# Performance work log

Hardware: AMD Instinct MI355X
Metric: run time of the kernel (lower is better)

Reference implementation:

```python
import jax, jax.numpy as jnp
import numpy as np

NUM_Q_HEADS = 64
NUM_KV_HEADS = 8
HEAD_DIM = 64
HIDDEN = 2880
SLIDING_WINDOW = 128
ROPE_WAVELENGTH = 10000.0
NEG_INF = jnp.float32(-1e9)


def _rope(x, start_index=0):
    # x: (b, s, n, h). yarn with scaling_factor=1.0 == standard RoPE (split-half rotate).
    s, h = x.shape[1], x.shape[-1]
    inv_freq = 1.0 / (ROPE_WAVELENGTH ** (jnp.arange(0, h, 2, dtype=jnp.float32) / h))
    pos = jnp.arange(s, dtype=jnp.float32) + start_index
    freqs = pos[:, None] * inv_freq[None, :]  # (s, h/2)
    cos = jnp.concatenate([jnp.cos(freqs), jnp.cos(freqs)], axis=-1)[None, :, None, :]
    sin = jnp.concatenate([jnp.sin(freqs), jnp.sin(freqs)], axis=-1)[None, :, None, :]
    x1, x2 = jnp.split(x, 2, axis=-1)
    rot = jnp.concatenate([-x2, x1], axis=-1)
    return x * cos + rot * sin


def setup_inputs() -> dict:
    key = jax.random.key(0)
    ks = jax.random.split(key, 9)
    b, s = 1, 2048
    scale = 0.02
    hidden_states = jax.random.normal(ks[0], (b, s, HIDDEN), jnp.float32)
    Wq = jax.random.normal(ks[1], (HIDDEN, NUM_Q_HEADS, HEAD_DIM), jnp.float32) * scale
    Wk = jax.random.normal(ks[2], (HIDDEN, NUM_KV_HEADS, HEAD_DIM), jnp.float32) * scale
    Wv = jax.random.normal(ks[3], (HIDDEN, NUM_KV_HEADS, HEAD_DIM), jnp.float32) * scale
    Wo = jax.random.normal(ks[4], (NUM_Q_HEADS, HEAD_DIM, HIDDEN), jnp.float32) * scale
    bq = jnp.zeros((NUM_Q_HEADS, HEAD_DIM), jnp.float32)
    bk = jnp.zeros((NUM_KV_HEADS, HEAD_DIM), jnp.float32)
    bv = jnp.zeros((NUM_KV_HEADS, HEAD_DIM), jnp.float32)
    bo = jnp.zeros((HIDDEN,), jnp.float32)
    sinks = jax.random.normal(ks[5], (NUM_Q_HEADS,), jnp.float32) * 0.05
    attention_mask = jnp.tril(jnp.ones((s, s), bool))[None]  # causal, (b, q, k)
    return dict(hidden_states=hidden_states, Wq=Wq, bq=bq, Wk=Wk, bk=bk, Wv=Wv,
                bv=bv, Wo=Wo, bo=bo, sinks=sinks, attention_mask=attention_mask)


def reference(hidden_states, Wq, bq, Wk, bk, Wv, bv, Wo, bo, sinks, attention_mask):
    b, s, _ = hidden_states.shape
    inv_norm = 1.0 / np.sqrt(HEAD_DIM).astype(np.float32)
    # QKV projections (EinsumDense with bias)
    q = jnp.einsum('bqm,muh->bquh', hidden_states, Wq) + bq
    k = jnp.einsum('bkm,mvh->bkvh', hidden_states, Wk) + bk
    v = jnp.einsum('bkm,mvh->bkvh', hidden_states, Wv) + bv
    # rotary_dim == head_dim (even), so RoPE applies to the full head dim
    q = _rope(q)
    k = _rope(k)
    # GQA: repeat kv heads
    groups = NUM_Q_HEADS // NUM_KV_HEADS
    k = jnp.repeat(k, groups, axis=2)
    v = jnp.repeat(v, groups, axis=2)
    scores = jnp.einsum('bquh,bkuh->buqk', q, k) * inv_norm
    # sliding-window mask: keep kv_pos >= q_pos - window
    qpos = jnp.arange(s)
    swin = qpos[None, :] >= qpos[:, None] - SLIDING_WINDOW  # (q, k)
    scores = jnp.where(swin[None, None], scores, NEG_INF)
    scores = jnp.where(attention_mask[:, None], scores, NEG_INF)
    # sink-token logit per head appended as extra kv column
    sink = jnp.broadcast_to(sinks.reshape(1, NUM_Q_HEADS, 1, 1), (b, NUM_Q_HEADS, s, 1))
    logits = jnp.concatenate([scores, sink], axis=-1)
    m = jax.lax.stop_gradient(jnp.max(logits, axis=-1, keepdims=True))
    probs = jax.nn.softmax(logits - m, axis=-1)[..., :-1]  # drop sink column
    attn = jnp.einsum('buqk,bkuh->bquh', probs, v)
    return jnp.einsum('bquh,uhm->bqm', attn, Wo) + bo
```

## Files before the change

### kernel.cpp

```cpp
#include <hip/hip_runtime.h>
#include <cstdint>

typedef __attribute__((ext_vector_type(4))) float f32x4;
typedef __attribute__((ext_vector_type(8))) short bf16x8;

#define HIDDEN 2880
#define SEQ 2048
#define QKV_N 5120
#define WIN 128

__device__ __forceinline__ ushort f2bf(float f) {
  uint32_t u = __builtin_bit_cast(uint32_t, f);
  u += 0x7fff + ((u >> 16) & 1);
  return (ushort)(u >> 16);
}
__device__ __forceinline__ float bf2f(ushort h) {
  uint32_t u = ((uint32_t)h) << 16;
  return __builtin_bit_cast(float, u);
}

__global__ void conv_kernel(const float* __restrict__ in, ushort* __restrict__ out, int n) {
  int i = (blockIdx.x * blockDim.x + threadIdx.x) * 4;
  if (i >= n) return;
  float4 v = *(const float4*)(in + i);
  ushort4 o;
  o.x = f2bf(v.x); o.y = f2bf(v.y); o.z = f2bf(v.z); o.w = f2bf(v.w);
  *(ushort4*)(out + i) = o;
}

__global__ __launch_bounds__(256) void tconv_kernel(const float* __restrict__ in, ushort* __restrict__ out,
                                                    int R, int C, int out_ld, int out_row_off) {
  __shared__ float tile[32][33];
  int c0 = blockIdx.x * 32, r0 = blockIdx.y * 32;
  int tx = threadIdx.x & 31, ty = threadIdx.x >> 5;
#pragma unroll
  for (int i = 0; i < 32; i += 8)
    tile[ty + i][tx] = in[(size_t)(r0 + ty + i) * C + c0 + tx];
  __syncthreads();
#pragma unroll
  for (int i = 0; i < 32; i += 8)
    out[(size_t)(out_row_off + c0 + ty + i) * out_ld + r0 + tx] = f2bf(tile[tx][ty + i]);
}

__global__ void biascat_kernel(const float* __restrict__ bq, const float* __restrict__ bk,
                               const float* __restrict__ bv, float* __restrict__ out) {
  int i = blockIdx.x * blockDim.x + threadIdx.x;
  if (i >= QKV_N) return;
  float v = (i < 4096) ? bq[i] : (i < 4608) ? bk[i - 4096] : bv[i - 4608];
  out[i] = v;
}

__global__ void ropetab_kernel(float2* __restrict__ tab) {
  int i = blockIdx.x * blockDim.x + threadIdx.x;
  int s = i >> 5, d = i & 31;
  float inv = powf(10000.0f, -(float)d / 32.0f);
  float f = (float)s * inv;
  tab[i] = make_float2(cosf(f), sinf(f));
}

__global__ void rope_kernel(ushort* __restrict__ buf, const float2* __restrict__ tab, int width, int total) {
  int idx = blockIdx.x * blockDim.x + threadIdx.x;
  if (idx >= total) return;
  int s = idx / width;
  int rr = idx - s * width;
  int d = rr & 63;
  ushort* p = buf + (size_t)s * QKV_N + rr;
  float x = bf2f(*p);
  float partner = __shfl_xor(x, 32, 64);
  float2 cs = tab[(s << 5) + (d & 31)];
  float o = x * cs.x + ((d < 32) ? -partner : partner) * cs.y;
  *p = f2bf(o);
}

__global__ __launch_bounds__(256) void vt_kernel(const ushort* __restrict__ qkv, ushort* __restrict__ vt) {
  __shared__ ushort tile[64][80];
  int kv0 = blockIdx.x * 64, d0 = blockIdx.y * 64;
  int t = threadIdx.x;
#pragma unroll
  for (int p = 0; p < 2; ++p) {
    int lr = p * 32 + (t >> 3);
    *(bf16x8*)&tile[lr][(t & 7) * 8] =
        *(const bf16x8*)&qkv[(size_t)(kv0 + lr) * QKV_N + 4608 + d0 + (t & 7) * 8];
  }
  __syncthreads();
#pragma unroll
  for (int p = 0; p < 2; ++p) {
    int dl = p * 32 + (t >> 3);
    bf16x8 o;
#pragma unroll
    for (int jj = 0; jj < 8; ++jj) o[jj] = (short)tile[(t & 7) * 8 + jj][dl];
    *(bf16x8*)&vt[(size_t)(d0 + dl) * 2048 + kv0 + (t & 7) * 8] = o;
  }
}

template <int BN, bool OUT_BF16>
__global__ __launch_bounds__(512, 2) void gemm8_kernel(
    const ushort* __restrict__ A, const ushort* __restrict__ Bt,
    const float* __restrict__ bias, void* __restrict__ Cv,
    int K, int lda, int ldb, int ldc) {
  constexpr int NFRAG = BN / 64;
  constexpr int BHALF = BN * 64;
  constexpr int BCHUNKS = BHALF / 1024;
  constexpr int BJ = BCHUNKS / 8, BR = BCHUNKS & 7;
  constexpr int BUFBYTES = 16384 + 2 * BHALF;
  __shared__ __align__(16) char ldsbuf[2 * BUFBYTES];

  const int cpx = gridDim.x >> 3;
  const int wg = ((int)blockIdx.x & 7) * cpx + ((int)blockIdx.x >> 3);
  const int mtile = wg & 15, ntile = wg >> 4;
  const int m0 = mtile * 128, n0 = ntile * BN;

  const int tid = threadIdx.x, wv = tid >> 6, l = tid & 63;
  const int wm = wv >> 2, wn = wv & 3;
  const int r = l & 15, g = l >> 4;

  const int c = l ^ ((l >> 3) & 3);
  const ushort* gA0 = A + (size_t)(m0 + wv * 16 + (c >> 2)) * lda + (c & 3) * 8;
  const ushort* gB0 = Bt + (size_t)(n0 + (c >> 2)) * ldb + (c & 3) * 8;

  const int gsw = (g * 16) ^ (((r >> 1) & 3) << 4);
  const int aOff = (wm * 64 + r) * 64 + gsw;
  const int bOff = (wn * NFRAG * 16 + r) * 64 + gsw;

  auto sA = [&](int nb, int kg, int kh) {
    __builtin_amdgcn_global_load_lds(
        (const __attribute__((address_space(1))) void*)(const void*)(gA0 + kg),
        (__attribute__((address_space(3))) void*)&ldsbuf[nb * BUFBYTES + kh * 8192 + wv * 1024], 16, 0, 0);
  };
  auto sB = [&](int nb, int kg, int kh) {
#pragma unroll
    for (int j = 0; j < (BCHUNKS + 7) / 8; ++j) {
      int cid = j * 8 + wv;
      if (cid < BCHUNKS)
        __builtin_amdgcn_global_load_lds(
            (const __attribute__((address_space(1))) void*)(const void*)(gB0 + (size_t)cid * 16 * ldb + kg),
            (__attribute__((address_space(3))) void*)&ldsbuf[nb * BUFBYTES + 16384 + kh * BHALF + cid * 1024],
            16, 0, 0);
    }
  };

#define BAR() __builtin_amdgcn_s_barrier()
#define LGKM0()                                              \
  do {                                                       \
    asm volatile("s_waitcnt lgkmcnt(0)" ::: "memory");       \
    __builtin_amdgcn_sched_barrier(0);                       \
  } while (0)
#define WAITVN()                                                                   \
  do {                                                                             \
    if (wv < BR) asm volatile("s_waitcnt vmcnt(%0)" ::"n"(BJ + 2) : "memory");     \
    else asm volatile("s_waitcnt vmcnt(%0)" ::"n"(BJ + 1) : "memory");             \
  } while (0)
#define WAITV0() asm volatile("s_waitcnt vmcnt(0)" ::: "memory")
#define READ_A(KH, MF0)                                                            \
  _Pragma("unroll") for (int i2 = 0; i2 < 2; ++i2)                                 \
      aq[i2] = *(const bf16x8*)&ldsbuf[bufOff + (KH)*8192 + aOff + ((MF0) + i2) * 1024];
#define READ_B(KH)                                                                 \
  _Pragma("unroll") for (int nf = 0; nf < NFRAG; ++nf)                             \
      bq[nf] = *(const bf16x8*)&ldsbuf[bufOff + 16384 + (KH)*BHALF + bOff + nf * 1024];
#define PHASE_MFMA(MB)                                                             \
  __builtin_amdgcn_s_setprio(1);                                                   \
  _Pragma("unroll") for (int i2 = 0; i2 < 2; ++i2) {                               \
    _Pragma("unroll") for (int nf = 0; nf < NFRAG; ++nf)                           \
        acc[(MB) + i2][nf] = __builtin_amdgcn_mfma_f32_16x16x32_bf16(              \
            aq[i2], bq[nf], acc[(MB) + i2][nf], 0, 0, 0);                          \
  }                                                                                \
  __builtin_amdgcn_s_setprio(0)

  f32x4 acc[4][NFRAG] = {};

  sA(0, 0, 0); sB(0, 0, 0); sA(0, 32, 1); sB(0, 32, 1);
  WAITVN();
  BAR();

  const int nt = K >> 6;
  for (int t = 0; t < nt; ++t) {
    const int buf = t & 1, nbuf = buf ^ 1;
    const int bufOff = buf * BUFBYTES;
    const int kn = (t + 1) << 6;
    const bool haveNext = (t + 1 < nt);
    bf16x8 aq[2], bq[NFRAG];

    READ_B(0); READ_A(0, 0);
    if (haveNext) sA(nbuf, kn, 0);
    BAR(); LGKM0();
    PHASE_MFMA(0);
    BAR();
    READ_A(0, 2);
    if (haveNext) { sB(nbuf, kn, 0); WAITVN(); } else { WAITV0(); }
    BAR(); LGKM0();
    PHASE_MFMA(2);
    BAR();
    READ_B(1); READ_A(1, 0);
    if (haveNext) sA(nbuf, kn + 32, 1);
    BAR(); LGKM0();
    PHASE_MFMA(0);
    BAR();
    READ_A(1, 2);
    if (haveNext) { sB(nbuf, kn + 32, 1); WAITVN(); } else { WAITV0(); }
    BAR(); LGKM0();
    PHASE_MFMA(2);
    BAR();
  }

#pragma unroll
  for (int mf2 = 0; mf2 < 4; ++mf2) {
#pragma unroll
    for (int nf = 0; nf < NFRAG; ++nf) {
      int cc = n0 + wn * (NFRAG * 16) + nf * 16 + r;
      float b = bias[cc];
#pragma unroll
      for (int j = 0; j < 4; ++j) {
        int rrow = m0 + wm * 64 + mf2 * 16 + g * 4 + j;
        float v = acc[mf2][nf][j] + b;
        if (OUT_BF16) ((ushort*)Cv)[(size_t)rrow * ldc + cc] = f2bf(v);
        else ((float*)Cv)[(size_t)rrow * ldc + cc] = v;
      }
    }
  }
#undef BAR
#undef LGKM0
#undef WAITVN
#undef WAITV0
#undef READ_A
#undef READ_B
#undef PHASE_MFMA
}

__global__ __launch_bounds__(512, 4) void attn_kernel(
    const ushort* __restrict__ qkv, const ushort* __restrict__ vt,
    const float* __restrict__ sinks, ushort* __restrict__ out) {
  __shared__ __align__(16) char lds[54272];
  const int kh = blockIdx.y;
  const int q0 = blockIdx.x * 32;
  const int kvw0 = q0 - 128;
  const int tid = threadIdx.x, w = tid >> 6, l = tid & 63;
  const int r = l & 15, g = l >> 4;
  const int h = kh * 8 + w;

  if (tid < 256) ((uint32_t*)(lds + 40960))[tid] = 0;

#pragma unroll
  for (int it = 0; it < 3; ++it) {
    int c = it * 512 + tid;
    if (c < 1280) {
      {
        int row = c >> 3, ch = c & 7;
        int kv = kvw0 + row;
        bf16x8 vv = {};
        if (kv >= 0) vv = *(const bf16x8*)&qkv[(size_t)kv * QKV_N + 4096 + kh * 64 + ch * 8];
        int byte = (row * 128 + ch * 16) ^ ((row & 7) << 4);
        *(bf16x8*)(lds + byte) = vv;
      }
      {
        int row = c / 20, ch = c - (c / 20) * 20;
        int kv = kvw0 + ch * 8;
        bf16x8 vv = {};
        if (kv >= 0) vv = *(const bf16x8*)&vt[(size_t)(kh * 64 + row) * 2048 + kv];
        int byte = (row * 320 + ch * 16) ^ ((row & 7) << 4);
        *(bf16x8*)(lds + 20480 + byte) = vv;
      }
    }
  }
  __syncthreads();

  char* Pw = lds + 41984 + w * 1536;
  const float snk = sinks[h];

#pragma unroll
  for (int si = 0; si < 2; ++si) {
    const ushort* qb = &qkv[(size_t)(q0 + si * 16 + r) * QKV_N + h * 64 + g * 8];
    bf16x8 qf0 = *(const bf16x8*)qb;
    bf16x8 qf1 = *(const bf16x8*)(qb + 32);

    f32x4 S[9];
    float mx[4] = {-3e30f, -3e30f, -3e30f, -3e30f};
#pragma unroll
    for (int tt = 0; tt < 9; ++tt) {
      int kvloc = (si + tt) * 16 + r;
      int b0 = (kvloc * 128 + g * 16) ^ ((kvloc & 7) << 4);
      int b1 = (kvloc * 128 + 64 + g * 16) ^ ((kvloc & 7) << 4);
      bf16x8 kf0 = *(const bf16x8*)(lds + b0);
      bf16x8 kf1 = *(const bf16x8*)(lds + b1);
      f32x4 s = {};
      s = __builtin_amdgcn_mfma_f32_16x16x32_bf16(qf0, kf0, s, 0, 0, 0);
      s = __builtin_amdgcn_mfma_f32_16x16x32_bf16(qf1, kf1, s, 0, 0, 0);
      int kvc = kvw0 + kvloc;
#pragma unroll
      for (int j = 0; j < 4; ++j) {
        int qr = q0 + si * 16 + g * 4 + j;
        bool valid = (kvc >= 0) && (kvc <= qr) && (kvc >= qr - WIN);
        float v = valid ? s[j] * 0.125f : -1e30f;
        s[j] = v;
        mx[j] = fmaxf(mx[j], v);
      }
      S[tt] = s;
    }
#pragma unroll
    for (int off = 1; off < 16; off <<= 1)
#pragma unroll
      for (int j = 0; j < 4; ++j) mx[j] = fmaxf(mx[j], __shfl_xor(mx[j], off, 64));
    float m[4], sum[4] = {0, 0, 0, 0};
#pragma unroll
    for (int j = 0; j < 4; ++j) m[j] = fmaxf(mx[j], snk);
#pragma unroll
    for (int tt = 0; tt < 9; ++tt)
#pragma unroll
      for (int j = 0; j < 4; ++j) {
        float p = (S[tt][j] > -1e29f) ? __expf(S[tt][j] - m[j]) : 0.0f;
        S[tt][j] = p;
        sum[j] += p;
      }
#pragma unroll
    for (int off = 1; off < 16; off <<= 1)
#pragma unroll
      for (int j = 0; j < 4; ++j) sum[j] += __shfl_xor(sum[j], off, 64);
    float rinv[4];
#pragma unroll
    for (int j = 0; j < 4; ++j) rinv[j] = 1.0f / (sum[j] + __expf(snk - m[j]));

    f32x4 acc[4] = {};
#pragma unroll
    for (int ks = 0; ks < 5; ++ks) {
#pragma unroll
      for (int c2 = 0; c2 < 2; ++c2) {
        int tt = 2 * ks + c2;
#pragma unroll
        for (int j = 0; j < 4; ++j) {
          float pv = (tt <= 8) ? S[tt][j] * rinv[j] : 0.0f;
          *(ushort*)(Pw + ((g * 4 + j) * 48 + c2 * 16 + r) * 2) = f2bf(pv);
        }
      }
      bf16x8 pa = *(const bf16x8*)(Pw + (r * 48 + g * 8) * 2);
#pragma unroll
      for (int ni = 0; ni < 4; ++ni) {
        int row = ni * 16 + r;
        int byte = (row * 320 + (si * 16 + ks * 32 + g * 8) * 2) ^ ((row & 7) << 4);
        bf16x8 vb = *(const bf16x8*)(lds + 20480 + byte);
        acc[ni] = __builtin_amdgcn_mfma_f32_16x16x32_bf16(pa, vb, acc[ni], 0, 0, 0);
      }
    }
#pragma unroll
    for (int ni = 0; ni < 4; ++ni)
#pragma unroll
      for (int j = 0; j < 4; ++j)
        out[(size_t)(q0 + si * 16 + g * 4 + j) * 4096 + h * 64 + ni * 16 + r] = f2bf(acc[ni][j]);
  }
}

extern "C" void kernel_launch(void* const* d_in, const int* in_sizes, int n_in,
                              void* d_out, int out_size, void* d_ws, size_t ws_size,
                              hipStream_t stream) {
  const float* hs = (const float*)d_in[0];
  const float* Wq = (const float*)d_in[1];
  const float* bq = (const float*)d_in[2];
  const float* Wk = (const float*)d_in[3];
  const float* bk = (const float*)d_in[4];
  const float* Wv = (const float*)d_in[5];
  const float* bv = (const float*)d_in[6];
  const float* Wo = (const float*)d_in[7];
  const float* bo = (const float*)d_in[8];
  const float* sinks = (const float*)d_in[9];
  float* out = (float*)d_out;

  char* ws = (char*)d_ws;
  ushort* hs_bf   = (ushort*)(ws + 0);
  ushort* vt_g    = (ushort*)(ws + 0);
  ushort* wqkv_t  = (ushort*)(ws + 11796480);
  ushort* attn    = (ushort*)(ws + 11796480);
  ushort* wo_t    = (ushort*)(ws + 41287680);
  ushort* qkv     = (ushort*)(ws + 66453504);
  float*  bias_all= (float*)(ws + 87425024);
  float2* tab     = (float2*)(ws + 87445504);

  conv_kernel<<<5898240 / 4 / 256, 256, 0, stream>>>(hs, hs_bf, 5898240);
  tconv_kernel<<<dim3(4096 / 32, 2880 / 32), 256, 0, stream>>>(Wq, wqkv_t, 2880, 4096, 2880, 0);
  tconv_kernel<<<dim3(512 / 32, 2880 / 32), 256, 0, stream>>>(Wk, wqkv_t, 2880, 512, 2880, 4096);
  tconv_kernel<<<dim3(512 / 32, 2880 / 32), 256, 0, stream>>>(Wv, wqkv_t, 2880, 512, 2880, 4608);
  tconv_kernel<<<dim3(2880 / 32, 4096 / 32), 256, 0, stream>>>(Wo, wo_t, 4096, 2880, 4096, 0);
  biascat_kernel<<<20, 256, 0, stream>>>(bq, bk, bv, bias_all);
  ropetab_kernel<<<2048 * 32 / 256, 256, 0, stream>>>(tab);

  gemm8_kernel<320, true><<<256, 512, 0, stream>>>(hs_bf, wqkv_t, bias_all, qkv,
                                                   2880, 2880, 2880, 5120);
  rope_kernel<<<8388608 / 256, 256, 0, stream>>>(qkv, tab, 4096, 8388608);
  rope_kernel<<<1048576 / 256, 256, 0, stream>>>(qkv + 4096, tab, 512, 1048576);
  vt_kernel<<<dim3(32, 8), 256, 0, stream>>>(qkv, vt_g);
  attn_kernel<<<dim3(64, 8), 512, 0, stream>>>(qkv, vt_g, sinks, attn);
  gemm8_kernel<192, false><<<240, 512, 0, stream>>>(attn, wo_t, bo, out,
                                                    4096, 4096, 4096, 2880);
}
```

Measured before the change: 214.9 us.

## Load GEMM A operand straight to registers and ring-buffer B through LDS

Both GEMMs now read the A operand straight from global memory into two register banks, double-buffered across k-tiles, instead of staging it in LDS. The B operand moves through a four-slot LDS ring that is prefetched two half-tiles ahead, with fewer barriers per k-step. The tile index mapping now takes an explicit N-tile count, which changes the block-to-tile order. This is meant to cut LDS traffic and synchronisation. In exchange, each wave sharing an M block reloads the same A rows from global memory, which adds L2 traffic and register pressure.

```diff
diff --git a/kernel.cpp b/kernel.cpp
--- a/kernel.cpp
+++ b/kernel.cpp
@@ -94,20 +94,20 @@
 }
 
 template <int BN, bool OUT_BF16>
-__global__ __launch_bounds__(512, 2) void gemm8_kernel(
+__global__ __launch_bounds__(512, 2) void gemm_ka_kernel(
     const ushort* __restrict__ A, const ushort* __restrict__ Bt,
     const float* __restrict__ bias, void* __restrict__ Cv,
-    int K, int lda, int ldb, int ldc) {
+    int K, int lda, int ldb, int ldc, int ntn) {
   constexpr int NFRAG = BN / 64;
-  constexpr int BHALF = BN * 64;
-  constexpr int BCHUNKS = BHALF / 1024;
-  constexpr int BJ = BCHUNKS / 8, BR = BCHUNKS & 7;
-  constexpr int BUFBYTES = 16384 + 2 * BHALF;
-  __shared__ __align__(16) char ldsbuf[2 * BUFBYTES];
+  constexpr int SLOT = BN * 64;
+  constexpr int CH = SLOT / 1024;
+  constexpr int CREM = CH & 7;
+  constexpr int CDIV = CH / 8;
+  __shared__ __align__(16) char lds[4 * SLOT];
 
   const int cpx = gridDim.x >> 3;
   const int wg = ((int)blockIdx.x & 7) * cpx + ((int)blockIdx.x >> 3);
-  const int mtile = wg & 15, ntile = wg >> 4;
+  const int mtile = wg / ntn, ntile = wg - mtile * ntn;
   const int m0 = mtile * 128, n0 = ntile * BN;
 
   const int tid = threadIdx.x, wv = tid >> 6, l = tid & 63;
@@ -115,91 +115,79 @@
   const int r = l & 15, g = l >> 4;
 
   const int c = l ^ ((l >> 3) & 3);
-  const ushort* gA0 = A + (size_t)(m0 + wv * 16 + (c >> 2)) * lda + (c & 3) * 8;
   const ushort* gB0 = Bt + (size_t)(n0 + (c >> 2)) * ldb + (c & 3) * 8;
-
+  const ushort* aG = A + (size_t)(m0 + wm * 64 + r) * lda + g * 8;
   const int gsw = (g * 16) ^ (((r >> 1) & 3) << 4);
-  const int aOff = (wm * 64 + r) * 64 + gsw;
-  const int bOff = (wn * NFRAG * 16 + r) * 64 + gsw;
-
-  auto sA = [&](int nb, int kg, int kh) {
-    __builtin_amdgcn_global_load_lds(
-        (const __attribute__((address_space(1))) void*)(const void*)(gA0 + kg),
-        (__attribute__((address_space(3))) void*)&ldsbuf[nb * BUFBYTES + kh * 8192 + wv * 1024], 16, 0, 0);
-  };
-  auto sB = [&](int nb, int kg, int kh) {
-#pragma unroll
-    for (int j = 0; j < (BCHUNKS + 7) / 8; ++j) {
+  const int bOff = (wn * (NFRAG * 16) + r) * 64 + gsw;
+
+  auto sB = [&](int slot, int kg) {
+#pragma unroll
+    for (int j = 0; j < (CH + 7) / 8; ++j) {
       int cid = j * 8 + wv;
-      if (cid < BCHUNKS)
+      if (cid < CH)
         __builtin_amdgcn_global_load_lds(
             (const __attribute__((address_space(1))) void*)(const void*)(gB0 + (size_t)cid * 16 * ldb + kg),
-            (__attribute__((address_space(3))) void*)&ldsbuf[nb * BUFBYTES + 16384 + kh * BHALF + cid * 1024],
-            16, 0, 0);
+            (__attribute__((address_space(3))) void*)&lds[slot * SLOT + cid * 1024], 16, 0, 0);
     }
   };
 
-#define BAR() __builtin_amdgcn_s_barrier()
-#define LGKM0()                                              \
-  do {                                                       \
-    asm volatile("s_waitcnt lgkmcnt(0)" ::: "memory");       \
-    __builtin_amdgcn_sched_barrier(0);                       \
+#define LOAD_A(BANK, KG)                                                           \
+  _Pragma("unroll") for (int kf = 0; kf < 8; ++kf)                                 \
+      BANK[kf] = *(const bf16x8*)(aG + (size_t)(kf & 3) * 16 * lda + (KG) + (kf >> 2) * 32);
+
+#define PHASE(SLOTI, BANK, KS)                                                     \
+  {                                                                                \
+    bf16x8 bq[NFRAG];                                                              \
+    _Pragma("unroll") for (int nf = 0; nf < NFRAG; ++nf)                           \
+        bq[nf] = *(const bf16x8*)&lds[(SLOTI)*SLOT + bOff + nf * 1024];            \
+    asm volatile("s_waitcnt lgkmcnt(0)" ::: "memory");                             \
+    __builtin_amdgcn_sched_barrier(0);                                             \
+    __builtin_amdgcn_s_setprio(1);                                                 \
+    _Pragma("unroll") for (int mi = 0; mi < 4; ++mi)                               \
+        _Pragma("unroll") for (int nf = 0; nf < NFRAG; ++nf)                       \
+            acc[mi][nf] = __builtin_amdgcn_mfma_f32_16x16x32_bf16(                 \
+                BANK[(KS)*4 + mi], bq[nf], acc[mi][nf], 0, 0, 0);                  \
+    __builtin_amdgcn_s_setprio(0);                                                 \
+  }
+
+#define WAITC()                                                                    \
+  do {                                                                             \
+    if (wv < CREM) asm volatile("s_waitcnt vmcnt(%0)" ::"n"(CDIV + 1) : "memory"); \
+    else asm volatile("s_waitcnt vmcnt(%0)" ::"n"(CDIV) : "memory");               \
   } while (0)
-#define WAITVN()                                                                   \
-  do {                                                                             \
-    if (wv < BR) asm volatile("s_waitcnt vmcnt(%0)" ::"n"(BJ + 2) : "memory");     \
-    else asm volatile("s_waitcnt vmcnt(%0)" ::"n"(BJ + 1) : "memory");             \
-  } while (0)
-#define WAITV0() asm volatile("s_waitcnt vmcnt(0)" ::: "memory")
-#define READ_A(KH, MF0)                                                            \
-  _Pragma("unroll") for (int i2 = 0; i2 < 2; ++i2)                                 \
-      aq[i2] = *(const bf16x8*)&ldsbuf[bufOff + (KH)*8192 + aOff + ((MF0) + i2) * 1024];
-#define READ_B(KH)                                                                 \
-  _Pragma("unroll") for (int nf = 0; nf < NFRAG; ++nf)                             \
-      bq[nf] = *(const bf16x8*)&ldsbuf[bufOff + 16384 + (KH)*BHALF + bOff + nf * 1024];
-#define PHASE_MFMA(MB)                                                             \
-  __builtin_amdgcn_s_setprio(1);                                                   \
-  _Pragma("unroll") for (int i2 = 0; i2 < 2; ++i2) {                               \
-    _Pragma("unroll") for (int nf = 0; nf < NFRAG; ++nf)                           \
-        acc[(MB) + i2][nf] = __builtin_amdgcn_mfma_f32_16x16x32_bf16(              \
-            aq[i2], bq[nf], acc[(MB) + i2][nf], 0, 0, 0);                          \
-  }                                                                                \
-  __builtin_amdgcn_s_setprio(0)
+
+#define TILE(T, S0, S1, SST1, SST2, CUR, NXT, DO_NXT)                              \
+  {                                                                                \
+    if (DO_NXT) {                                                                  \
+      sB(SST1, ((T) + 1) * 64 + 32);                                               \
+      LOAD_A(NXT, ((T) + 1) * 64);                                                 \
+    }                                                                              \
+    PHASE(S0, CUR, 0);                                                             \
+    __builtin_amdgcn_s_barrier();                                                  \
+    if ((T) + 2 < nt) sB(SST2, ((T) + 2) * 64);                                    \
+    PHASE(S1, CUR, 1);                                                             \
+    WAITC();                                                                       \
+    __builtin_amdgcn_s_barrier();                                                  \
+  }
 
   f32x4 acc[4][NFRAG] = {};
-
-  sA(0, 0, 0); sB(0, 0, 0); sA(0, 32, 1); sB(0, 32, 1);
-  WAITVN();
-  BAR();
-
+  bf16x8 a0[8], a1[8];
   const int nt = K >> 6;
-  for (int t = 0; t < nt; ++t) {
-    const int buf = t & 1, nbuf = buf ^ 1;
-    const int bufOff = buf * BUFBYTES;
-    const int kn = (t + 1) << 6;
-    const bool haveNext = (t + 1 < nt);
-    bf16x8 aq[2], bq[NFRAG];
-
-    READ_B(0); READ_A(0, 0);
-    if (haveNext) sA(nbuf, kn, 0);
-    BAR(); LGKM0();
-    PHASE_MFMA(0);
-    BAR();
-    READ_A(0, 2);
-    if (haveNext) { sB(nbuf, kn, 0); WAITVN(); } else { WAITV0(); }
-    BAR(); LGKM0();
-    PHASE_MFMA(2);
-    BAR();
-    READ_B(1); READ_A(1, 0);
-    if (haveNext) sA(nbuf, kn + 32, 1);
-    BAR(); LGKM0();
-    PHASE_MFMA(0);
-    BAR();
-    READ_A(1, 2);
-    if (haveNext) { sB(nbuf, kn + 32, 1); WAITVN(); } else { WAITV0(); }
-    BAR(); LGKM0();
-    PHASE_MFMA(2);
-    BAR();
+
+  sB(0, 0); sB(1, 32); sB(2, 64);
+  LOAD_A(a0, 0);
+  asm volatile("s_waitcnt vmcnt(0)" ::: "memory");
+  __builtin_amdgcn_s_barrier();
+
+  int t = 0;
+  for (; t + 1 < nt; t += 2) {
+    TILE(t, 0, 1, 3, 0, a0, a1, true);
+    TILE(t + 1, 2, 3, 1, 2, a1, a0, (t + 2 < nt));
+  }
+  if (t < nt) {
+    PHASE(0, a0, 0);
+    __builtin_amdgcn_s_barrier();
+    PHASE(1, a0, 1);
   }
 
 #pragma unroll
@@ -217,13 +205,10 @@
       }
     }
   }
-#undef BAR
-#undef LGKM0
-#undef WAITVN
-#undef WAITV0
-#undef READ_A
-#undef READ_B
-#undef PHASE_MFMA
+#undef LOAD_A
+#undef PHASE
+#undef WAITC
+#undef TILE
 }
 
 __global__ __launch_bounds__(512, 4) void attn_kernel(
@@ -380,12 +365,12 @@
   biascat_kernel<<<20, 256, 0, stream>>>(bq, bk, bv, bias_all);
   ropetab_kernel<<<2048 * 32 / 256, 256, 0, stream>>>(tab);
 
-  gemm8_kernel<320, true><<<256, 512, 0, stream>>>(hs_bf, wqkv_t, bias_all, qkv,
-                                                   2880, 2880, 2880, 5120);
+  gemm_ka_kernel<320, true><<<256, 512, 0, stream>>>(hs_bf, wqkv_t, bias_all, qkv,
+                                                     2880, 2880, 2880, 5120, 16);
   rope_kernel<<<8388608 / 256, 256, 0, stream>>>(qkv, tab, 4096, 8388608);
   rope_kernel<<<1048576 / 256, 256, 0, stream>>>(qkv + 4096, tab, 512, 1048576);
   vt_kernel<<<dim3(32, 8), 256, 0, stream>>>(qkv, vt_g);
   attn_kernel<<<dim3(64, 8), 512, 0, stream>>>(qkv, vt_g, sinks, attn);
-  gemm8_kernel<192, false><<<240, 512, 0, stream>>>(attn, wo_t, bo, out,
-                                                    4096, 4096, 4096, 2880);
-}
+  gemm_ka_kernel<192, false><<<240, 512, 0, stream>>>(attn, wo_t, bo, out,
+                                                      4096, 4096, 4096, 2880, 15);
+}
```

Result: slower. 370.7 us (+72.5%).

## Simplify GEMM main loop to one-stage prefetch with single barrier per tile

Applied to the files above, without the earlier changes.

Replaces the four-phase interleaved GEMM loop, which had several barriers and partial vmcnt waits, with a simpler loop. Each iteration issues all next-tile global-to-LDS loads up front, then runs two k-halves of LDS reads and MFMAs, then waits for all loads and takes one barrier. Launch-bound occupancy becomes a template parameter, and the output projection GEMM is set to 4 waves-min. This cuts barrier and synchronisation overhead per tile but loses fine-grained overlap and doubles A fragments held in registers. The higher occupancy target may also force register spills or be unreachable given the LDS footprint.

```diff
diff --git a/kernel.cpp b/kernel.cpp
--- a/kernel.cpp
+++ b/kernel.cpp
@@ -93,15 +93,14 @@
   }
 }
 
-template <int BN, bool OUT_BF16>
-__global__ __launch_bounds__(512, 2) void gemm8_kernel(
+template <int BN, bool OUT_BF16, int MINW>
+__global__ __launch_bounds__(512, MINW) void gemm8_kernel(
     const ushort* __restrict__ A, const ushort* __restrict__ Bt,
     const float* __restrict__ bias, void* __restrict__ Cv,
     int K, int lda, int ldb, int ldc) {
   constexpr int NFRAG = BN / 64;
   constexpr int BHALF = BN * 64;
   constexpr int BCHUNKS = BHALF / 1024;
-  constexpr int BJ = BCHUNKS / 8, BR = BCHUNKS & 7;
   constexpr int BUFBYTES = 16384 + 2 * BHALF;
   __shared__ __align__(16) char ldsbuf[2 * BUFBYTES];
 
@@ -120,7 +119,7 @@
 
   const int gsw = (g * 16) ^ (((r >> 1) & 3) << 4);
   const int aOff = (wm * 64 + r) * 64 + gsw;
-  const int bOff = (wn * NFRAG * 16 + r) * 64 + gsw;
+  const int bOff = (wn * (NFRAG * 16) + r) * 64 + gsw;
 
   auto sA = [&](int nb, int kg, int kh) {
     __builtin_amdgcn_global_load_lds(
@@ -145,60 +144,42 @@
     asm volatile("s_waitcnt lgkmcnt(0)" ::: "memory");       \
     __builtin_amdgcn_sched_barrier(0);                       \
   } while (0)
-#define WAITVN()                                                                   \
-  do {                                                                             \
-    if (wv < BR) asm volatile("s_waitcnt vmcnt(%0)" ::"n"(BJ + 2) : "memory");     \
-    else asm volatile("s_waitcnt vmcnt(%0)" ::"n"(BJ + 1) : "memory");             \
-  } while (0)
 #define WAITV0() asm volatile("s_waitcnt vmcnt(0)" ::: "memory")
-#define READ_A(KH, MF0)                                                            \
-  _Pragma("unroll") for (int i2 = 0; i2 < 2; ++i2)                                 \
-      aq[i2] = *(const bf16x8*)&ldsbuf[bufOff + (KH)*8192 + aOff + ((MF0) + i2) * 1024];
-#define READ_B(KH)                                                                 \
-  _Pragma("unroll") for (int nf = 0; nf < NFRAG; ++nf)                             \
-      bq[nf] = *(const bf16x8*)&ldsbuf[bufOff + 16384 + (KH)*BHALF + bOff + nf * 1024];
-#define PHASE_MFMA(MB)                                                             \
-  __builtin_amdgcn_s_setprio(1);                                                   \
-  _Pragma("unroll") for (int i2 = 0; i2 < 2; ++i2) {                               \
-    _Pragma("unroll") for (int nf = 0; nf < NFRAG; ++nf)                           \
-        acc[(MB) + i2][nf] = __builtin_amdgcn_mfma_f32_16x16x32_bf16(              \
-            aq[i2], bq[nf], acc[(MB) + i2][nf], 0, 0, 0);                          \
-  }                                                                                \
-  __builtin_amdgcn_s_setprio(0)
 
   f32x4 acc[4][NFRAG] = {};
-
-  sA(0, 0, 0); sB(0, 0, 0); sA(0, 32, 1); sB(0, 32, 1);
-  WAITVN();
+  const int nt = K >> 6;
+
+  sA(0, 0, 0); sA(0, 32, 1); sB(0, 0, 0); sB(0, 32, 1);
+  WAITV0();
   BAR();
 
-  const int nt = K >> 6;
   for (int t = 0; t < nt; ++t) {
-    const int buf = t & 1, nbuf = buf ^ 1;
-    const int bufOff = buf * BUFBYTES;
-    const int kn = (t + 1) << 6;
-    const bool haveNext = (t + 1 < nt);
-    bf16x8 aq[2], bq[NFRAG];
-
-    READ_B(0); READ_A(0, 0);
-    if (haveNext) sA(nbuf, kn, 0);
-    BAR(); LGKM0();
-    PHASE_MFMA(0);
-    BAR();
-    READ_A(0, 2);
-    if (haveNext) { sB(nbuf, kn, 0); WAITVN(); } else { WAITV0(); }
-    BAR(); LGKM0();
-    PHASE_MFMA(2);
-    BAR();
-    READ_B(1); READ_A(1, 0);
-    if (haveNext) sA(nbuf, kn + 32, 1);
-    BAR(); LGKM0();
-    PHASE_MFMA(0);
-    BAR();
-    READ_A(1, 2);
-    if (haveNext) { sB(nbuf, kn + 32, 1); WAITVN(); } else { WAITV0(); }
-    BAR(); LGKM0();
-    PHASE_MFMA(2);
+    const int bufOff = (t & 1) * BUFBYTES;
+    const int nb = (t & 1) ^ 1;
+    if (t + 1 < nt) {
+      const int kn = (t + 1) * 64;
+      sA(nb, kn, 0); sA(nb, kn + 32, 1);
+      sB(nb, kn, 0); sB(nb, kn + 32, 1);
+    }
+#pragma unroll
+    for (int kh = 0; kh < 2; ++kh) {
+      bf16x8 aq[4], bq[NFRAG];
+#pragma unroll
+      for (int nf = 0; nf < NFRAG; ++nf)
+        bq[nf] = *(const bf16x8*)&ldsbuf[bufOff + 16384 + kh * BHALF + bOff + nf * 1024];
+#pragma unroll
+      for (int mi = 0; mi < 4; ++mi)
+        aq[mi] = *(const bf16x8*)&ldsbuf[bufOff + kh * 8192 + aOff + mi * 1024];
+      LGKM0();
+      __builtin_amdgcn_s_setprio(1);
+#pragma unroll
+      for (int mi = 0; mi < 4; ++mi)
+#pragma unroll
+        for (int nf = 0; nf < NFRAG; ++nf)
+          acc[mi][nf] = __builtin_amdgcn_mfma_f32_16x16x32_bf16(aq[mi], bq[nf], acc[mi][nf], 0, 0, 0);
+      __builtin_amdgcn_s_setprio(0);
+    }
+    WAITV0();
     BAR();
   }
 
@@ -219,11 +200,7 @@
   }
 #undef BAR
 #undef LGKM0
-#undef WAITVN
 #undef WAITV0
-#undef READ_A
-#undef READ_B
-#undef PHASE_MFMA
 }
 
 __global__ __launch_bounds__(512, 4) void attn_kernel(
@@ -380,12 +357,12 @@
   biascat_kernel<<<20, 256, 0, stream>>>(bq, bk, bv, bias_all);
   ropetab_kernel<<<2048 * 32 / 256, 256, 0, stream>>>(tab);
 
-  gemm8_kernel<320, true><<<256, 512, 0, stream>>>(hs_bf, wqkv_t, bias_all, qkv,
-                                                   2880, 2880, 2880, 5120);
+  gemm8_kernel<320, true, 2><<<256, 512, 0, stream>>>(hs_bf, wqkv_t, bias_all, qkv,
+                                                      2880, 2880, 2880, 5120);
   rope_kernel<<<8388608 / 256, 256, 0, stream>>>(qkv, tab, 4096, 8388608);
   rope_kernel<<<1048576 / 256, 256, 0, stream>>>(qkv + 4096, tab, 512, 1048576);
   vt_kernel<<<dim3(32, 8), 256, 0, stream>>>(qkv, vt_g);
   attn_kernel<<<dim3(64, 8), 512, 0, stream>>>(qkv, vt_g, sinks, attn);
-  gemm8_kernel<192, false><<<240, 512, 0, stream>>>(attn, wo_t, bo, out,
-                                                    4096, 4096, 4096, 2880);
-}
+  gemm8_kernel<192, false, 4><<<240, 512, 0, stream>>>(attn, wo_t, bo, out,
+                                                       4096, 4096, 4096, 2880);
+}
```

Measured after the change: 212.2 us. No clear change (-1.3%).
